# Kernel tuning notes

Measured on AMD Instinct MI355X. Metric: run time of the kernel, lower is better.

Reference implementation:

```python
import jax, jax.numpy as jnp
import numpy as np
import math

HIDDEN = 256
NUM_GAUSSIANS = 64
NUM_FILTERS = 256
CUTOFF = 1.0
COSINE_OFFSET = 0.0
N_NODES = 10000
N_EDGES = 320000


def ssp(x):
    # shifted softplus: softplus(x) - log(2)
    return jax.nn.softplus(x) - jnp.log(2.0).astype(x.dtype)


def setup_inputs() -> dict:
    key = jax.random.key(0)
    ks = jax.random.split(key, 12)

    def xavier(k, fan_out, fan_in):
        a = math.sqrt(6.0 / (fan_in + fan_out))
        return jax.random.uniform(k, (fan_out, fan_in), jnp.float32, -a, a)

    x = jax.random.normal(ks[0], (N_NODES, HIDDEN), jnp.float32)
    ji_pairs = jax.random.randint(ks[1], (2, N_EDGES), 0, N_NODES, jnp.int64)
    e_ji = jax.random.uniform(ks[2], (N_EDGES,), jnp.float32)  # distances in [0, cutoff)
    e_ji_basis = jax.random.normal(ks[3], (N_EDGES, NUM_GAUSSIANS), jnp.float32)

    return {
        "x": x,
        "ji_pairs": ji_pairs,
        "e_ji": e_ji,
        "e_ji_basis": e_ji_basis,
        # filter_nn: Linear(G->F), ssp, Linear(F->F)
        "fw1": xavier(ks[4], NUM_FILTERS, NUM_GAUSSIANS),
        "fb1": jnp.zeros((NUM_FILTERS,), jnp.float32),
        "fw2": xavier(ks[5], NUM_FILTERS, NUM_FILTERS),
        "fb2": jnp.zeros((NUM_FILTERS,), jnp.float32),
        # CFConv linears
        "w1": xavier(ks[6], NUM_FILTERS, HIDDEN),            # linear1, no bias
        "w2": xavier(ks[7], HIDDEN, NUM_FILTERS),            # linear2
        "b2": jnp.zeros((HIDDEN,), jnp.float32),
        # linear3
        "w3": xavier(ks[8], HIDDEN, HIDDEN),
        "b3": jnp.zeros((HIDDEN,), jnp.float32),
    }


def reference(x, ji_pairs, e_ji, e_ji_basis, fw1, fb1, fw2, fb2, w1, w2, b2, w3, b3):
    pi = jnp.asarray(math.pi, x.dtype)
    # cosine cutoff: C = 0.25 * (cos((e - off) * pi / (cutoff - off)) + 1)
    C = 0.25 * (jnp.cos((e_ji - COSINE_OFFSET) * pi / (CUTOFF - COSINE_OFFSET)) + 1.0)
    # filter network on edge RBF features: [E, F]
    W = ssp(e_ji_basis @ fw1.T + fb1) @ fw2.T + fb2
    W = W * C[:, None]
    # linear1 (no bias): [N, F]
    h = x @ w1.T
    # message: x_j * W, gathered from source nodes ji_pairs[0]
    src, dst = ji_pairs[0], ji_pairs[1]
    msg = h[src] * W                                   # [E, F]
    agg = jax.ops.segment_sum(msg, dst, num_segments=x.shape[0])  # [N, F]
    # linear2
    out = agg @ w2.T + b2
    # interaction block tail: act + linear3
    out = ssp(out) @ w3.T + b3
    return out
```

## Files before the change

kernel.cpp:

```cpp
#include <hip/hip_runtime.h>
#include <hip/hip_bf16.h>

typedef __bf16 bf16_t;
typedef float f32x4 __attribute__((ext_vector_type(4)));
typedef __bf16 bf16x8 __attribute__((ext_vector_type(8)));

#define NNODES 10000
#define NEDGES 320000
#define NPAD   10048
#define NPB    8
#define NBLK   (NPAD / NPB)

#define OFF_AGG   256
#define OFF_JIN   (OFF_AGG  + (size_t)NPAD * 256 * 4)
#define OFF_HIST  (OFF_JIN  + (size_t)2 * NEDGES * 4)
#define OFF_CUR   (OFF_HIST + 10240 * 4)
#define OFF_CSR   (OFF_CUR  + 10240 * 4)
#define OFF_PERM  (OFF_CSR  + 10240 * 4)
#define OFF_SRCS  (OFF_PERM + (size_t)NEDGES * 4)
#define OFF_DSTS  (OFF_SRCS + (size_t)NEDGES * 4)
#define OFF_CES   (OFF_DSTS + (size_t)NEDGES * 4)
#define OFF_CE    (OFF_CES  + (size_t)NEDGES * 4)
#define OFF_WB    (OFF_CE   + (size_t)NEDGES * 4)
#define FW1B 0
#define FW2B 16384
#define W1B  81920
#define W2B  147456
#define W3B  212992
#define FB1B 278528
#define FB2B 278784
#define B2B  279040
#define B3B  279296
#define WBN  279552
#define WS_NEED (OFF_WB + (size_t)WBN * 2)
#define OFF_BASC  ((WS_NEED + 255) & ~(size_t)255)
#define WS_NEED_BIG (OFF_BASC + (size_t)NEDGES * 64 * 2)

__device__ __forceinline__ float ssp_f(float v) {
    return fmaxf(v, 0.f) + __logf(1.f + __expf(-fabsf(v))) - 0.69314718055994531f;
}
__device__ __forceinline__ f32x4 mfma16(bf16x8 a, bf16x8 b, f32x4 c) {
    return __builtin_amdgcn_mfma_f32_16x16x32_bf16(a, b, c, 0, 0, 0);
}
template<bool ISB>
__device__ __forceinline__ bf16x8 ld8(const void* p, size_t off) {
    if constexpr (ISB) return *(const bf16x8*)((const bf16_t*)p + off);
    else {
        const float* f = (const float*)p + off;
        f32x4 lo = *(const f32x4*)f, hi = *(const f32x4*)(f + 4);
        bf16x8 r;
        for (int j = 0; j < 4; ++j) { r[j] = (bf16_t)lo[j]; r[j + 4] = (bf16_t)hi[j]; }
        return r;
    }
}
__device__ __forceinline__ bf16x8 ld8r(bool isb, const void* p, size_t off) {
    if (isb) return *(const bf16x8*)((const bf16_t*)p + off);
    const float* f = (const float*)p + off;
    f32x4 lo = *(const f32x4*)f, hi = *(const f32x4*)(f + 4);
    bf16x8 r;
    for (int j = 0; j < 4; ++j) { r[j] = (bf16_t)lo[j]; r[j + 4] = (bf16_t)hi[j]; }
    return r;
}
template<bool ISB>
__device__ __forceinline__ void st1(void* p, size_t off, float v) {
    if constexpr (ISB) ((bf16_t*)p)[off] = (bf16_t)v;
    else               ((float*)p)[off] = v;
}
__device__ __forceinline__ float ld1r(bool isb, const void* p, size_t off) {
    return isb ? (float)((const bf16_t*)p)[off] : ((const float*)p)[off];
}

__global__ __launch_bounds__(256) void detect_kernel(
    const void* __restrict__ x, const int* __restrict__ jraw,
    int* __restrict__ flags, int* __restrict__ hist)
{
    __shared__ int cnt, hi;
    if (threadIdx.x == 0) { cnt = 0; hi = 0; }
    __syncthreads();
    const unsigned short* xw = (const unsigned short*)x;
    int local = 0;
    for (int i = threadIdx.x; i < 2048; i += 256) {
        unsigned int e = (xw[2 * i] >> 7) & 0xFF;
        if (e >= 100 && e <= 141) local++;
    }
    atomicAdd(&cnt, local);
    int v = 0;
    for (int i = threadIdx.x; i < 1024; i += 256) v |= jraw[2 * i + 1];
    if (v != 0) atomicOr(&hi, 1);
    for (int i = threadIdx.x; i < 10240; i += 256) hist[i] = 0;
    __syncthreads();
    if (threadIdx.x == 0) { flags[0] = (cnt > 1024) ? 1 : 0; flags[1] = (hi == 0) ? 1 : 0; }
}

__global__ __launch_bounds__(256) void prep_kernel(
    const int* __restrict__ raw, const int* __restrict__ flags,
    const void* __restrict__ e_ji, const void* __restrict__ basis,
    const void* fw1, const void* fb1, const void* fw2, const void* fb2,
    const void* w1, const void* w2, const void* b2, const void* w3, const void* b3,
    int* __restrict__ jin, int* __restrict__ hist, float* __restrict__ ce,
    bf16_t* __restrict__ wb, bf16_t* __restrict__ basc, int doconv)
{
    const bool is64 = (flags[1] != 0);
    const bool isb  = (flags[0] != 0);
    const int gid = blockIdx.x * 256 + threadIdx.x;
    if (gid < 2 * NEDGES) {
        int iv = is64 ? raw[2 * gid] : raw[gid];
        iv = iv < 0 ? 0 : (iv >= NNODES ? NNODES - 1 : iv);
        jin[gid] = iv;
        if (gid >= NEDGES) atomicAdd(&hist[iv], 1);
    }
    if (gid < NEDGES)
        ce[gid] = 0.25f * (cosf(3.14159265358979f * ld1r(isb, e_ji, gid)) + 1.0f);
    if (gid < WBN) {
        int g = gid; const void* s; int so;
        if      (g < FW2B) { s = fw1; so = g - FW1B; }
        else if (g < W1B)  { s = fw2; so = g - FW2B; }
        else if (g < W2B)  { s = w1;  so = g - W1B; }
        else if (g < W3B)  { s = w2;  so = g - W2B; }
        else if (g < FB1B) { s = w3;  so = g - W3B; }
        else if (g < FB2B) { s = fb1; so = g - FB1B; }
        else if (g < B2B)  { s = fb2; so = g - FB2B; }
        else if (g < B3B)  { s = b2;  so = g - B2B; }
        else               { s = b3;  so = g - B3B; }
        wb[gid] = (bf16_t)ld1r(isb, s, so);
    }
    if (doconv) {
        const int nv = NEDGES * 64 / 8;
        for (int i = gid; i < nv; i += gridDim.x * 256)
            ((bf16x8*)basc)[i] = ld8r(isb, basis, (size_t)i * 8);
    }
}

__global__ __launch_bounds__(256) void scan_kernel(
    const int* __restrict__ hist, int* __restrict__ cur, int* __restrict__ csr)
{
    __shared__ int s[256];
    const int t = threadIdx.x;
    int loc[40]; int sum = 0;
    const int base = t * 40;
    for (int j = 0; j < 40; ++j) {
        int i = base + j;
        loc[j] = (i < NNODES) ? hist[i] : 0;
        sum += loc[j];
    }
    s[t] = sum; __syncthreads();
    for (int off = 1; off < 256; off <<= 1) {
        int v = (t >= off) ? s[t - off] : 0;
        __syncthreads();
        if (t >= off) s[t] += v;
        __syncthreads();
    }
    int pre = (t == 0) ? 0 : s[t - 1];
    for (int j = 0; j < 40; ++j) {
        int i = base + j;
        cur[i] = pre;
        csr[i] = pre;
        pre += loc[j];
    }
}

__global__ __launch_bounds__(256) void scatter_kernel(
    const int* __restrict__ jin, const float* __restrict__ ce,
    int* __restrict__ cur, int* __restrict__ perm,
    int* __restrict__ src_s, int* __restrict__ dst_s, float* __restrict__ ce_s)
{
    int e = blockIdx.x * 256 + threadIdx.x;
    if (e < NEDGES) {
        int d = jin[NEDGES + e];
        int pos = atomicAdd(&cur[d], 1);
        perm[pos]  = e;
        src_s[pos] = jin[e];
        dst_s[pos] = d;
        ce_s[pos]  = ce[e];
    }
}

template<bool ISB>
__global__ __launch_bounds__(256, 2) void h_gemm_kernel(
    const void* __restrict__ x, const bf16_t* __restrict__ wb,
    bf16_t* __restrict__ h, const int* __restrict__ flags)
{
    if ((flags[0] != 0) != ISB) return;
    const bf16_t* w1b = wb + W1B;
    const int w = threadIdx.x >> 6, L = threadIdx.x & 63;
    const int lane16 = L & 15, quad = L >> 4;
    const int nb = blockIdx.x * 64, cb = w * 64;
    f32x4 acc[4][4] = {};
    for (int kc = 0; kc < 8; ++kc) {
        const int ko = kc * 32 + quad * 8;
        bf16x8 af[4], bfr[4];
        for (int mt = 0; mt < 4; ++mt) {
            int row = nb + mt * 16 + lane16;
            if (row >= NNODES) row = NNODES - 1;
            af[mt] = ld8<ISB>(x, (size_t)row * 256 + ko);
        }
        for (int nt = 0; nt < 4; ++nt)
            bfr[nt] = *(const bf16x8*)(w1b + (size_t)(cb + nt * 16 + lane16) * 256 + ko);
        for (int mt = 0; mt < 4; ++mt)
            for (int nt = 0; nt < 4; ++nt)
                acc[mt][nt] = mfma16(af[mt], bfr[nt], acc[mt][nt]);
    }
    for (int mt = 0; mt < 4; ++mt)
        for (int r = 0; r < 4; ++r) {
            int row = nb + mt * 16 + quad * 4 + r;
            if (row < NNODES)
                for (int nt = 0; nt < 4; ++nt)
                    h[(size_t)row * 256 + cb + nt * 16 + lane16] = (bf16_t)acc[mt][nt][r];
        }
}

template<bool ISB, bool CONV>
__global__ __launch_bounds__(256, 3) void edge_kernel(
    const void* __restrict__ basis, const int* __restrict__ csr,
    const int* __restrict__ perm, const int* __restrict__ src_s,
    const int* __restrict__ dst_s, const float* __restrict__ ce_s,
    const bf16_t* __restrict__ wb, const bf16_t* __restrict__ h,
    float* __restrict__ agg, const int* __restrict__ flags)
{
    if (!CONV && (flags[0] != 0) != ISB) return;
    __shared__ bf16_t T[64][264];
    __shared__ float G[NPB][260];
    __shared__ int sperm[64], ssrc[64], snrow[64];
    __shared__ float sce[64];
    const int tid = threadIdx.x;
    const int w = tid >> 6, L = tid & 63;
    const int lane16 = L & 15, quad = L >> 4;
    const int cb = w * 64;
    const int nbase  = blockIdx.x * NPB;
    const int estart = csr[nbase];
    const int eend   = csr[nbase + NPB];

    for (int i = tid; i < NPB * 260; i += 256) (&G[0][0])[i] = 0.f;

    const bf16_t* fw1b = wb + FW1B;
    const bf16_t* fw2b = wb + FW2B;
    float fb1v[4], fb2v[4];
    for (int nt = 0; nt < 4; ++nt) {
        fb1v[nt] = (float)wb[FB1B + cb + nt * 16 + lane16];
        fb2v[nt] = (float)wb[FB2B + cb + nt * 16 + lane16];
    }

    const int hrow = tid >> 2, hseg = tid & 3;

    for (int e0 = estart & ~63; e0 < eend; e0 += 64) {
        __syncthreads();
        {
            int g = tid >> 6, i = tid & 63;
            int e = e0 + i;
            bool valid = (e >= estart) && (e < eend);
            int ee = valid ? e : estart;
            if      (g == 0) sperm[i] = perm[ee];
            else if (g == 1) ssrc[i] = src_s[ee];
            else if (g == 2) {
                int nr = dst_s[ee] - nbase;
                snrow[i] = nr < 0 ? 0 : (nr > NPB - 1 ? NPB - 1 : nr);
            }
            else sce[i] = valid ? ce_s[ee] : 0.f;
        }
        __syncthreads();

        bf16x8 hreg[8];
        {
            const bf16_t* hs = h + (size_t)ssrc[hrow] * 256 + hseg * 64;
            #pragma unroll
            for (int j = 0; j < 8; ++j) hreg[j] = ((const bf16x8*)hs)[j];
        }

        int prow[4];
        for (int mt = 0; mt < 4; ++mt) prow[mt] = sperm[mt * 16 + lane16];

        f32x4 acc1[4][4] = {};
        for (int kc = 0; kc < 2; ++kc) {
            const int ko = kc * 32 + quad * 8;
            bf16x8 af[4], bfr[4];
            for (int mt = 0; mt < 4; ++mt)
                af[mt] = ld8<CONV ? true : ISB>(basis, (size_t)prow[mt] * 64 + ko);
            for (int nt = 0; nt < 4; ++nt)
                bfr[nt] = *(const bf16x8*)(fw1b + (size_t)(cb + nt * 16 + lane16) * 64 + ko);
            for (int mt = 0; mt < 4; ++mt)
                for (int nt = 0; nt < 4; ++nt)
                    acc1[mt][nt] = mfma16(af[mt], bfr[nt], acc1[mt][nt]);
        }
        for (int nt = 0; nt < 4; ++nt) {
            int col = cb + nt * 16 + lane16;
            for (int mt = 0; mt < 4; ++mt)
                for (int r = 0; r < 4; ++r)
                    T[mt * 16 + quad * 4 + r][col] = (bf16_t)ssp_f(acc1[mt][nt][r] + fb1v[nt]);
        }
        __syncthreads();

        f32x4 acc2[4][4] = {};
        for (int kc = 0; kc < 8; ++kc) {
            const int ko = kc * 32 + quad * 8;
            bf16x8 af[4], bfr[4];
            for (int mt = 0; mt < 4; ++mt)
                af[mt] = *(const bf16x8*)(&T[mt * 16 + lane16][ko]);
            for (int nt = 0; nt < 4; ++nt)
                bfr[nt] = *(const bf16x8*)(fw2b + (size_t)(cb + nt * 16 + lane16) * 256 + ko);
            for (int mt = 0; mt < 4; ++mt)
                for (int nt = 0; nt < 4; ++nt)
                    acc2[mt][nt] = mfma16(af[mt], bfr[nt], acc2[mt][nt]);
        }
        __syncthreads();

        {
            bf16_t* dp = &T[hrow][hseg * 64];
            #pragma unroll
            for (int j = 0; j < 8; ++j) ((bf16x8*)dp)[j] = hreg[j];
        }
        __syncthreads();

        float run[4] = {0, 0, 0, 0};
        int curn = -1;
        for (int mt = 0; mt < 4; ++mt)
            for (int r = 0; r < 4; ++r) {
                int row = mt * 16 + quad * 4 + r;
                int nr = snrow[row];
                if (nr != curn) {
                    if (curn >= 0)
                        for (int nt = 0; nt < 4; ++nt)
                            atomicAdd(&G[curn][cb + nt * 16 + lane16], run[nt]);
                    curn = nr;
                    run[0] = run[1] = run[2] = run[3] = 0.f;
                }
                float cv = sce[row];
                for (int nt = 0; nt < 4; ++nt) {
                    int col = cb + nt * 16 + lane16;
                    run[nt] += (acc2[mt][nt][r] + fb2v[nt]) * cv * (float)T[row][col];
                }
            }
        if (curn >= 0)
            for (int nt = 0; nt < 4; ++nt)
                atomicAdd(&G[curn][cb + nt * 16 + lane16], run[nt]);
    }
    __syncthreads();

    for (int n = 0; n < NPB; ++n)
        agg[(size_t)(nbase + n) * 256 + tid] = G[n][tid];
}

template<bool ISB>
__global__ __launch_bounds__(256, 2) void out_kernel(
    const float* __restrict__ agg, const bf16_t* __restrict__ wb,
    void* __restrict__ out, const int* __restrict__ flags)
{
    if ((flags[0] != 0) != ISB) return;
    const bf16_t* w2b = wb + W2B;
    const bf16_t* w3b = wb + W3B;
    __shared__ bf16_t U[64][264];
    const int w = threadIdx.x >> 6, L = threadIdx.x & 63;
    const int lane16 = L & 15, quad = L >> 4;
    const int nb = blockIdx.x * 64, cb = w * 64;

    f32x4 acc[4][4] = {};
    for (int kc = 0; kc < 8; ++kc) {
        const int ko = kc * 32 + quad * 8;
        bf16x8 af[4], bfr[4];
        for (int mt = 0; mt < 4; ++mt) {
            int row = nb + mt * 16 + lane16;
            const float* p = agg + (size_t)row * 256 + ko;
            f32x4 lo = *(const f32x4*)p, hi = *(const f32x4*)(p + 4);
            bf16x8 a;
            for (int j = 0; j < 4; ++j) { a[j] = (bf16_t)lo[j]; a[j + 4] = (bf16_t)hi[j]; }
            af[mt] = a;
        }
        for (int nt = 0; nt < 4; ++nt)
            bfr[nt] = *(const bf16x8*)(w2b + (size_t)(cb + nt * 16 + lane16) * 256 + ko);
        for (int mt = 0; mt < 4; ++mt)
            for (int nt = 0; nt < 4; ++nt)
                acc[mt][nt] = mfma16(af[mt], bfr[nt], acc[mt][nt]);
    }
    for (int nt = 0; nt < 4; ++nt) {
        int col = cb + nt * 16 + lane16;
        float bias = (float)wb[B2B + col];
        for (int mt = 0; mt < 4; ++mt)
            for (int r = 0; r < 4; ++r)
                U[mt * 16 + quad * 4 + r][col] = (bf16_t)ssp_f(acc[mt][nt][r] + bias);
    }
    __syncthreads();

    f32x4 acc2[4][4] = {};
    for (int kc = 0; kc < 8; ++kc) {
        const int ko = kc * 32 + quad * 8;
        bf16x8 af[4], bfr[4];
        for (int mt = 0; mt < 4; ++mt)
            af[mt] = *(const bf16x8*)(&U[mt * 16 + lane16][ko]);
        for (int nt = 0; nt < 4; ++nt)
            bfr[nt] = *(const bf16x8*)(w3b + (size_t)(cb + nt * 16 + lane16) * 256 + ko);
        for (int mt = 0; mt < 4; ++mt)
            for (int nt = 0; nt < 4; ++nt)
                acc2[mt][nt] = mfma16(af[mt], bfr[nt], acc2[mt][nt]);
    }
    for (int mt = 0; mt < 4; ++mt)
        for (int r = 0; r < 4; ++r) {
            int row = nb + mt * 16 + quad * 4 + r;
            if (row < NNODES)
                for (int nt = 0; nt < 4; ++nt) {
                    int col = cb + nt * 16 + lane16;
                    st1<ISB>(out, (size_t)row * 256 + col,
                             acc2[mt][nt][r] + (float)wb[B3B + col]);
                }
        }
}

extern "C" void kernel_launch(void* const* d_in, const int* in_sizes, int n_in,
                              void* d_out, int out_size, void* d_ws, size_t ws_size,
                              hipStream_t stream) {
    const void* x     = d_in[0];
    const int*  ji    = (const int*)d_in[1];
    const void* e_ji  = d_in[2];
    const void* basis = d_in[3];
    const void* fw1   = d_in[4];
    const void* fb1   = d_in[5];
    const void* fw2   = d_in[6];
    const void* fb2   = d_in[7];
    const void* w1    = d_in[8];
    const void* w2    = d_in[9];
    const void* b2    = d_in[10];
    const void* w3    = d_in[11];
    const void* b3    = d_in[12];

    if (ws_size < WS_NEED) return;
    const bool bigws = ws_size >= WS_NEED_BIG;

    char* W = (char*)d_ws;
    int*    flags = (int*)W;
    float*  agg   = (float*)(W + OFF_AGG);
    int*    jin   = (int*)(W + OFF_JIN);
    int*    hist  = (int*)(W + OFF_HIST);
    int*    cur   = (int*)(W + OFF_CUR);
    int*    csr   = (int*)(W + OFF_CSR);
    int*    perm  = (int*)(W + OFF_PERM);
    int*    src_s = (int*)(W + OFF_SRCS);
    int*    dst_s = (int*)(W + OFF_DSTS);
    float*  ce_s  = (float*)(W + OFF_CES);
    float*  ce    = (float*)(W + OFF_CE);
    bf16_t* wb    = (bf16_t*)(W + OFF_WB);
    bf16_t* basc  = (bf16_t*)(W + OFF_BASC);
    bf16_t* h     = (bf16_t*)d_out;

    detect_kernel<<<1, 256, 0, stream>>>(x, ji, flags, hist);
    prep_kernel<<<2500, 256, 0, stream>>>(ji, flags, e_ji, basis, fw1, fb1, fw2, fb2,
                                          w1, w2, b2, w3, b3, jin, hist, ce, wb,
                                          basc, bigws ? 1 : 0);
    scan_kernel<<<1, 256, 0, stream>>>(hist, cur, csr);
    scatter_kernel<<<1250, 256, 0, stream>>>(jin, ce, cur, perm, src_s, dst_s, ce_s);
    h_gemm_kernel<true ><<<157, 256, 0, stream>>>(x, wb, h, flags);
    h_gemm_kernel<false><<<157, 256, 0, stream>>>(x, wb, h, flags);
    if (bigws) {
        edge_kernel<true, true><<<NBLK, 256, 0, stream>>>(basc, csr, perm, src_s, dst_s, ce_s, wb, h, agg, flags);
    } else {
        edge_kernel<true,  false><<<NBLK, 256, 0, stream>>>(basis, csr, perm, src_s, dst_s, ce_s, wb, h, agg, flags);
        edge_kernel<false, false><<<NBLK, 256, 0, stream>>>(basis, csr, perm, src_s, dst_s, ce_s, wb, h, agg, flags);
    }
    out_kernel<true ><<<157, 256, 0, stream>>>(agg, wb, d_out, flags);
    out_kernel<false><<<157, 256, 0, stream>>>(agg, wb, d_out, flags);
}
```

Baseline: 583.7 us.

## Store basis in dst-sorted order and prefetch next edge tile in edge kernel

The scatter kernel now writes the bf16 basis rows in CSR (destination-sorted) order, replacing the separate conversion pass in prep. A new edge_fast_kernel reads those rows contiguously instead of gathering them through perm. It also software-prefetches the next 64-edge tile's basis, src index, dst row, cutoff and h rows into registers while the current tile computes. Each block now handles 16 nodes instead of 8, and blocks with no edges exit early. The costs are higher register pressure, and the scatter's per-edge 128-byte writes land at scattered positions.

New measurement: 633.2 us. 8.5% more time.

```diff
diff --git a/kernel.cpp b/kernel.cpp
--- a/kernel.cpp
+++ b/kernel.cpp
@@ -10,6 +10,8 @@
 #define NPAD   10048
 #define NPB    8
 #define NBLK   (NPAD / NPB)
+#define NPBE   16
+#define NBLKE  (NPAD / NPBE)
 
 #define OFF_AGG   256
 #define OFF_JIN   (OFF_AGG  + (size_t)NPAD * 256 * 4)
@@ -34,7 +36,7 @@
 #define WBN  279552
 #define WS_NEED (OFF_WB + (size_t)WBN * 2)
 #define OFF_BASC  ((WS_NEED + 255) & ~(size_t)255)
-#define WS_NEED_BIG (OFF_BASC + (size_t)NEDGES * 64 * 2)
+#define WS_NEED_BIG (OFF_BASC + (size_t)(NEDGES + 64) * 64 * 2)
 
 __device__ __forceinline__ float ssp_f(float v) {
     return fmaxf(v, 0.f) + __logf(1.f + __expf(-fabsf(v))) - 0.69314718055994531f;
@@ -94,11 +96,11 @@
 
 __global__ __launch_bounds__(256) void prep_kernel(
     const int* __restrict__ raw, const int* __restrict__ flags,
-    const void* __restrict__ e_ji, const void* __restrict__ basis,
+    const void* __restrict__ e_ji,
     const void* fw1, const void* fb1, const void* fw2, const void* fb2,
     const void* w1, const void* w2, const void* b2, const void* w3, const void* b3,
     int* __restrict__ jin, int* __restrict__ hist, float* __restrict__ ce,
-    bf16_t* __restrict__ wb, bf16_t* __restrict__ basc, int doconv)
+    bf16_t* __restrict__ wb)
 {
     const bool is64 = (flags[1] != 0);
     const bool isb  = (flags[0] != 0);
@@ -124,11 +126,6 @@
         else               { s = b3;  so = g - B3B; }
         wb[gid] = (bf16_t)ld1r(isb, s, so);
     }
-    if (doconv) {
-        const int nv = NEDGES * 64 / 8;
-        for (int i = gid; i < nv; i += gridDim.x * 256)
-            ((bf16x8*)basc)[i] = ld8r(isb, basis, (size_t)i * 8);
-    }
 }
 
 __global__ __launch_bounds__(256) void scan_kernel(
@@ -161,17 +158,31 @@
 
 __global__ __launch_bounds__(256) void scatter_kernel(
     const int* __restrict__ jin, const float* __restrict__ ce,
+    const void* __restrict__ basis, const int* __restrict__ flags,
     int* __restrict__ cur, int* __restrict__ perm,
-    int* __restrict__ src_s, int* __restrict__ dst_s, float* __restrict__ ce_s)
+    int* __restrict__ src_s, int* __restrict__ dst_s, float* __restrict__ ce_s,
+    bf16_t* __restrict__ basc, int doconv)
 {
     int e = blockIdx.x * 256 + threadIdx.x;
-    if (e < NEDGES) {
-        int d = jin[NEDGES + e];
-        int pos = atomicAdd(&cur[d], 1);
-        perm[pos]  = e;
-        src_s[pos] = jin[e];
-        dst_s[pos] = d;
-        ce_s[pos]  = ce[e];
+    if (e >= NEDGES) return;
+    int d = jin[NEDGES + e];
+    int pos = atomicAdd(&cur[d], 1);
+    perm[pos]  = e;
+    src_s[pos] = jin[e];
+    dst_s[pos] = d;
+    ce_s[pos]  = ce[e];
+    if (doconv) {
+        const bool isb = (flags[0] != 0);
+        bf16_t* dp = basc + (size_t)pos * 64;
+        if (isb) {
+            #pragma unroll
+            for (int j = 0; j < 8; ++j)
+                *(bf16x8*)(dp + j * 8) = *(const bf16x8*)((const bf16_t*)basis + (size_t)e * 64 + j * 8);
+        } else {
+            #pragma unroll
+            for (int j = 0; j < 8; ++j)
+                *(bf16x8*)(dp + j * 8) = ld8r(false, basis, (size_t)e * 64 + j * 8);
+        }
     }
 }
 
@@ -209,28 +220,33 @@
         }
 }
 
-template<bool ISB, bool CONV>
-__global__ __launch_bounds__(256, 3) void edge_kernel(
-    const void* __restrict__ basis, const int* __restrict__ csr,
-    const int* __restrict__ perm, const int* __restrict__ src_s,
-    const int* __restrict__ dst_s, const float* __restrict__ ce_s,
+__global__ __launch_bounds__(256, 3) void edge_fast_kernel(
+    const bf16_t* __restrict__ basc, const int* __restrict__ csr,
+    const int* __restrict__ src_s, const int* __restrict__ dst_s,
+    const float* __restrict__ ce_s,
     const bf16_t* __restrict__ wb, const bf16_t* __restrict__ h,
-    float* __restrict__ agg, const int* __restrict__ flags)
-{
-    if (!CONV && (flags[0] != 0) != ISB) return;
+    float* __restrict__ agg)
+{
     __shared__ bf16_t T[64][264];
-    __shared__ float G[NPB][260];
-    __shared__ int sperm[64], ssrc[64], snrow[64];
+    __shared__ float G[NPBE][260];
+    __shared__ int snrow[64];
     __shared__ float sce[64];
     const int tid = threadIdx.x;
     const int w = tid >> 6, L = tid & 63;
     const int lane16 = L & 15, quad = L >> 4;
     const int cb = w * 64;
-    const int nbase  = blockIdx.x * NPB;
+    const int nbase  = blockIdx.x * NPBE;
     const int estart = csr[nbase];
-    const int eend   = csr[nbase + NPB];
-
-    for (int i = tid; i < NPB * 260; i += 256) (&G[0][0])[i] = 0.f;
+    const int eend   = csr[nbase + NPBE];
+
+    for (int i = tid; i < NPBE * 260; i += 256) (&G[0][0])[i] = 0.f;
+
+    if (estart >= eend) {
+        __syncthreads();
+        for (int n = 0; n < NPBE; ++n)
+            agg[(size_t)(nbase + n) * 256 + tid] = 0.f;
+        return;
+    }
 
     const bf16_t* fw1b = wb + FW1B;
     const bf16_t* fw2b = wb + FW2B;
@@ -241,51 +257,79 @@
     }
 
     const int hrow = tid >> 2, hseg = tid & 3;
-
-    for (int e0 = estart & ~63; e0 < eend; e0 += 64) {
-        __syncthreads();
-        {
-            int g = tid >> 6, i = tid & 63;
-            int e = e0 + i;
+    const int e0first = estart & ~63;
+
+    int mrow = 0; float mce = 0.f; int msrc;
+    bf16x8 breg[2][4];
+    bf16x8 hreg[8];
+
+    {
+        int e = e0first + L;
+        int ec = e < NEDGES - 1 ? e : NEDGES - 1;
+        if (w == 0) {
             bool valid = (e >= estart) && (e < eend);
-            int ee = valid ? e : estart;
-            if      (g == 0) sperm[i] = perm[ee];
-            else if (g == 1) ssrc[i] = src_s[ee];
-            else if (g == 2) {
-                int nr = dst_s[ee] - nbase;
-                snrow[i] = nr < 0 ? 0 : (nr > NPB - 1 ? NPB - 1 : nr);
+            int nr = dst_s[ec] - nbase;
+            mrow = nr < 0 ? 0 : (nr > NPBE - 1 ? NPBE - 1 : nr);
+            mce  = valid ? ce_s[ec] : 0.f;
+        }
+        int eh = e0first + hrow; eh = eh < NEDGES - 1 ? eh : NEDGES - 1;
+        msrc = src_s[eh];
+        #pragma unroll
+        for (int kc = 0; kc < 2; ++kc)
+            #pragma unroll
+            for (int mt = 0; mt < 4; ++mt) {
+                int er = e0first + mt * 16 + lane16;
+                er = er < NEDGES - 1 ? er : NEDGES - 1;
+                breg[kc][mt] = *(const bf16x8*)(basc + (size_t)er * 64 + kc * 32 + quad * 8);
             }
-            else sce[i] = valid ? ce_s[ee] : 0.f;
-        }
-        __syncthreads();
-
-        bf16x8 hreg[8];
-        {
-            const bf16_t* hs = h + (size_t)ssrc[hrow] * 256 + hseg * 64;
-            #pragma unroll
-            for (int j = 0; j < 8; ++j) hreg[j] = ((const bf16x8*)hs)[j];
-        }
-
-        int prow[4];
-        for (int mt = 0; mt < 4; ++mt) prow[mt] = sperm[mt * 16 + lane16];
+        const bf16_t* hs = h + (size_t)msrc * 256 + hseg * 64;
+        #pragma unroll
+        for (int j = 0; j < 8; ++j) hreg[j] = ((const bf16x8*)hs)[j];
+    }
+
+    for (int e0 = e0first; e0 < eend; e0 += 64) {
+        const int e0n = e0 + 64;
+        const bool more = e0n < eend;
+        __syncthreads();
+        if (w == 0) { snrow[L] = mrow; sce[L] = mce; }
 
         f32x4 acc1[4][4] = {};
+        #pragma unroll
         for (int kc = 0; kc < 2; ++kc) {
             const int ko = kc * 32 + quad * 8;
-            bf16x8 af[4], bfr[4];
-            for (int mt = 0; mt < 4; ++mt)
-                af[mt] = ld8<CONV ? true : ISB>(basis, (size_t)prow[mt] * 64 + ko);
+            bf16x8 bfr[4];
             for (int nt = 0; nt < 4; ++nt)
                 bfr[nt] = *(const bf16x8*)(fw1b + (size_t)(cb + nt * 16 + lane16) * 64 + ko);
             for (int mt = 0; mt < 4; ++mt)
                 for (int nt = 0; nt < 4; ++nt)
-                    acc1[mt][nt] = mfma16(af[mt], bfr[nt], acc1[mt][nt]);
+                    acc1[mt][nt] = mfma16(breg[kc][mt], bfr[nt], acc1[mt][nt]);
         }
         for (int nt = 0; nt < 4; ++nt) {
             int col = cb + nt * 16 + lane16;
             for (int mt = 0; mt < 4; ++mt)
                 for (int r = 0; r < 4; ++r)
                     T[mt * 16 + quad * 4 + r][col] = (bf16_t)ssp_f(acc1[mt][nt][r] + fb1v[nt]);
+        }
+
+        if (more) {
+            int e = e0n + L;
+            int ec = e < NEDGES - 1 ? e : NEDGES - 1;
+            if (w == 0) {
+                bool valid = e < eend;
+                int nr = dst_s[ec] - nbase;
+                mrow = nr < 0 ? 0 : (nr > NPBE - 1 ? NPBE - 1 : nr);
+                mce  = valid ? ce_s[ec] : 0.f;
+            }
+            int eh = e0n + hrow; eh = eh < NEDGES - 1 ? eh : NEDGES - 1;
+            msrc = src_s[eh];
+            #pragma unroll
+            for (int kc = 0; kc < 2; ++kc)
+                #pragma unroll
+                for (int mt = 0; mt < 4; ++mt) {
+                    int er = e0n + mt * 16 + lane16;
+                    er = er < NEDGES - 1 ? er : NEDGES - 1;
+                    breg[kc][mt] = *(const bf16x8*)(basc + (size_t)er * 64 + kc * 32 + quad * 8);
+                }
         }
         __syncthreads();
 
@@ -309,6 +353,12 @@
             for (int j = 0; j < 8; ++j) ((bf16x8*)dp)[j] = hreg[j];
         }
         __syncthreads();
+
+        if (more) {
+            const bf16_t* hs = h + (size_t)msrc * 256 + hseg * 64;
+            #pragma unroll
+            for (int j = 0; j < 8; ++j) hreg[j] = ((const bf16x8*)hs)[j];
+        }
 
         float run[4] = {0, 0, 0, 0};
         int curn = -1;
@@ -335,6 +385,136 @@
     }
     __syncthreads();
 
+    for (int n = 0; n < NPBE; ++n)
+        agg[(size_t)(nbase + n) * 256 + tid] = G[n][tid];
+}
+
+template<bool ISB>
+__global__ __launch_bounds__(256, 3) void edge_kernel(
+    const void* __restrict__ basis, const int* __restrict__ csr,
+    const int* __restrict__ perm, const int* __restrict__ src_s,
+    const int* __restrict__ dst_s, const float* __restrict__ ce_s,
+    const bf16_t* __restrict__ wb, const bf16_t* __restrict__ h,
+    float* __restrict__ agg, const int* __restrict__ flags)
+{
+    if ((flags[0] != 0) != ISB) return;
+    __shared__ bf16_t T[64][264];
+    __shared__ float G[NPB][260];
+    __shared__ int sperm[64], ssrc[64], snrow[64];
+    __shared__ float sce[64];
+    const int tid = threadIdx.x;
+    const int w = tid >> 6, L = tid & 63;
+    const int lane16 = L & 15, quad = L >> 4;
+    const int cb = w * 64;
+    const int nbase  = blockIdx.x * NPB;
+    const int estart = csr[nbase];
+    const int eend   = csr[nbase + NPB];
+
+    for (int i = tid; i < NPB * 260; i += 256) (&G[0][0])[i] = 0.f;
+
+    const bf16_t* fw1b = wb + FW1B;
+    const bf16_t* fw2b = wb + FW2B;
+    float fb1v[4], fb2v[4];
+    for (int nt = 0; nt < 4; ++nt) {
+        fb1v[nt] = (float)wb[FB1B + cb + nt * 16 + lane16];
+        fb2v[nt] = (float)wb[FB2B + cb + nt * 16 + lane16];
+    }
+
+    const int hrow = tid >> 2, hseg = tid & 3;
+
+    for (int e0 = estart & ~63; e0 < eend; e0 += 64) {
+        __syncthreads();
+        {
+            int g = tid >> 6, i = tid & 63;
+            int e = e0 + i;
+            bool valid = (e >= estart) && (e < eend);
+            int ee = valid ? e : estart;
+            if      (g == 0) sperm[i] = perm[ee];
+            else if (g == 1) ssrc[i] = src_s[ee];
+            else if (g == 2) {
+                int nr = dst_s[ee] - nbase;
+                snrow[i] = nr < 0 ? 0 : (nr > NPB - 1 ? NPB - 1 : nr);
+            }
+            else sce[i] = valid ? ce_s[ee] : 0.f;
+        }
+        __syncthreads();
+
+        bf16x8 hreg[8];
+        {
+            const bf16_t* hs = h + (size_t)ssrc[hrow] * 256 + hseg * 64;
+            #pragma unroll
+            for (int j = 0; j < 8; ++j) hreg[j] = ((const bf16x8*)hs)[j];
+        }
+
+        int prow[4];
+        for (int mt = 0; mt < 4; ++mt) prow[mt] = sperm[mt * 16 + lane16];
+
+        f32x4 acc1[4][4] = {};
+        for (int kc = 0; kc < 2; ++kc) {
+            const int ko = kc * 32 + quad * 8;
+            bf16x8 af[4], bfr[4];
+            for (int mt = 0; mt < 4; ++mt)
+                af[mt] = ld8<ISB>(basis, (size_t)prow[mt] * 64 + ko);
+            for (int nt = 0; nt < 4; ++nt)
+                bfr[nt] = *(const bf16x8*)(fw1b + (size_t)(cb + nt * 16 + lane16) * 64 + ko);
+            for (int mt = 0; mt < 4; ++mt)
+                for (int nt = 0; nt < 4; ++nt)
+                    acc1[mt][nt] = mfma16(af[mt], bfr[nt], acc1[mt][nt]);
+        }
+        for (int nt = 0; nt < 4; ++nt) {
+            int col = cb + nt * 16 + lane16;
+            for (int mt = 0; mt < 4; ++mt)
+                for (int r = 0; r < 4; ++r)
+                    T[mt * 16 + quad * 4 + r][col] = (bf16_t)ssp_f(acc1[mt][nt][r] + fb1v[nt]);
+        }
+        __syncthreads();
+
+        f32x4 acc2[4][4] = {};
+        for (int kc = 0; kc < 8; ++kc) {
+            const int ko = kc * 32 + quad * 8;
+            bf16x8 af[4], bfr[4];
+            for (int mt = 0; mt < 4; ++mt)
+                af[mt] = *(const bf16x8*)(&T[mt * 16 + lane16][ko]);
+            for (int nt = 0; nt < 4; ++nt)
+                bfr[nt] = *(const bf16x8*)(fw2b + (size_t)(cb + nt * 16 + lane16) * 256 + ko);
+            for (int mt = 0; mt < 4; ++mt)
+                for (int nt = 0; nt < 4; ++nt)
+                    acc2[mt][nt] = mfma16(af[mt], bfr[nt], acc2[mt][nt]);
+        }
+        __syncthreads();
+
+        {
+            bf16_t* dp = &T[hrow][hseg * 64];
+            #pragma unroll
+            for (int j = 0; j < 8; ++j) ((bf16x8*)dp)[j] = hreg[j];
+        }
+        __syncthreads();
+
+        float run[4] = {0, 0, 0, 0};
+        int curn = -1;
+        for (int mt = 0; mt < 4; ++mt)
+            for (int r = 0; r < 4; ++r) {
+                int row = mt * 16 + quad * 4 + r;
+                int nr = snrow[row];
+                if (nr != curn) {
+                    if (curn >= 0)
+                        for (int nt = 0; nt < 4; ++nt)
+                            atomicAdd(&G[curn][cb + nt * 16 + lane16], run[nt]);
+                    curn = nr;
+                    run[0] = run[1] = run[2] = run[3] = 0.f;
+                }
+                float cv = sce[row];
+                for (int nt = 0; nt < 4; ++nt) {
+                    int col = cb + nt * 16 + lane16;
+                    run[nt] += (acc2[mt][nt][r] + fb2v[nt]) * cv * (float)T[row][col];
+                }
+            }
+        if (curn >= 0)
+            for (int nt = 0; nt < 4; ++nt)
+                atomicAdd(&G[curn][cb + nt * 16 + lane16], run[nt]);
+    }
+    __syncthreads();
+
     for (int n = 0; n < NPB; ++n)
         agg[(size_t)(nbase + n) * 256 + tid] = G[n][tid];
 }
@@ -440,18 +620,18 @@
     bf16_t* h     = (bf16_t*)d_out;
 
     detect_kernel<<<1, 256, 0, stream>>>(x, ji, flags, hist);
-    prep_kernel<<<2500, 256, 0, stream>>>(ji, flags, e_ji, basis, fw1, fb1, fw2, fb2,
-                                          w1, w2, b2, w3, b3, jin, hist, ce, wb,
-                                          basc, bigws ? 1 : 0);
+    prep_kernel<<<2500, 256, 0, stream>>>(ji, flags, e_ji, fw1, fb1, fw2, fb2,
+                                          w1, w2, b2, w3, b3, jin, hist, ce, wb);
     scan_kernel<<<1, 256, 0, stream>>>(hist, cur, csr);
-    scatter_kernel<<<1250, 256, 0, stream>>>(jin, ce, cur, perm, src_s, dst_s, ce_s);
+    scatter_kernel<<<1250, 256, 0, stream>>>(jin, ce, basis, flags, cur, perm,
+                                             src_s, dst_s, ce_s, basc, bigws ? 1 : 0);
     h_gemm_kernel<true ><<<157, 256, 0, stream>>>(x, wb, h, flags);
     h_gemm_kernel<false><<<157, 256, 0, stream>>>(x, wb, h, flags);
     if (bigws) {
-        edge_kernel<true, true><<<NBLK, 256, 0, stream>>>(basc, csr, perm, src_s, dst_s, ce_s, wb, h, agg, flags);
+        edge_fast_kernel<<<NBLKE, 256, 0, stream>>>(basc, csr, src_s, dst_s, ce_s, wb, h, agg);
     } else {
-        edge_kernel<true,  false><<<NBLK, 256, 0, stream>>>(basis, csr, perm, src_s, dst_s, ce_s, wb, h, agg, flags);
-        edge_kernel<false, false><<<NBLK, 256, 0, stream>>>(basis, csr, perm, src_s, dst_s, ce_s, wb, h, agg, flags);
+        edge_kernel<true ><<<NBLK, 256, 0, stream>>>(basis, csr, perm, src_s, dst_s, ce_s, wb, h, agg, flags);
+        edge_kernel<false><<<NBLK, 256, 0, stream>>>(basis, csr, perm, src_s, dst_s, ce_s, wb, h, agg, flags);
     }
     out_kernel<true ><<<157, 256, 0, stream>>>(agg, wb, d_out, flags);
     out_kernel<false><<<157, 256, 0, stream>>>(agg, wb, d_out, flags);
```

## Parallelize edge kernel over fixed 64-edge chunks with global atomics

Applied to the files above, without the earlier changes.

The edge kernel no longer gives each block a group of 8 destination nodes that it walks through edge tile by edge tile. Each block now handles exactly one 64-edge tile of the dst-sorted edge list and adds run-length partial sums straight into global agg with atomics. agg is now zeroed in prep_kernel, and the bf16 pre-conversion of the basis into a workspace copy is removed. This evens out load across blocks, removes the per-block loop, the shared accumulator and the partial-tile waste, and raises occupancy to 4 blocks. The cost is global float atomics on contention at node boundaries and always reading the basis in its original format.

Result: faster. 525.8 us (-9.9%).

```diff
diff --git a/kernel.cpp b/kernel.cpp
--- a/kernel.cpp
+++ b/kernel.cpp
@@ -8,8 +8,7 @@
 #define NNODES 10000
 #define NEDGES 320000
 #define NPAD   10048
-#define NPB    8
-#define NBLK   (NPAD / NPB)
+#define NB2    (NEDGES / 64)
 
 #define OFF_AGG   256
 #define OFF_JIN   (OFF_AGG  + (size_t)NPAD * 256 * 4)
@@ -33,8 +32,6 @@
 #define B3B  279296
 #define WBN  279552
 #define WS_NEED (OFF_WB + (size_t)WBN * 2)
-#define OFF_BASC  ((WS_NEED + 255) & ~(size_t)255)
-#define WS_NEED_BIG (OFF_BASC + (size_t)NEDGES * 64 * 2)
 
 __device__ __forceinline__ float ssp_f(float v) {
     return fmaxf(v, 0.f) + __logf(1.f + __expf(-fabsf(v))) - 0.69314718055994531f;
@@ -53,14 +50,6 @@
         return r;
     }
 }
-__device__ __forceinline__ bf16x8 ld8r(bool isb, const void* p, size_t off) {
-    if (isb) return *(const bf16x8*)((const bf16_t*)p + off);
-    const float* f = (const float*)p + off;
-    f32x4 lo = *(const f32x4*)f, hi = *(const f32x4*)(f + 4);
-    bf16x8 r;
-    for (int j = 0; j < 4; ++j) { r[j] = (bf16_t)lo[j]; r[j + 4] = (bf16_t)hi[j]; }
-    return r;
-}
 template<bool ISB>
 __device__ __forceinline__ void st1(void* p, size_t off, float v) {
     if constexpr (ISB) ((bf16_t*)p)[off] = (bf16_t)v;
@@ -94,11 +83,11 @@
 
 __global__ __launch_bounds__(256) void prep_kernel(
     const int* __restrict__ raw, const int* __restrict__ flags,
-    const void* __restrict__ e_ji, const void* __restrict__ basis,
+    const void* __restrict__ e_ji,
     const void* fw1, const void* fb1, const void* fw2, const void* fb2,
     const void* w1, const void* w2, const void* b2, const void* w3, const void* b3,
     int* __restrict__ jin, int* __restrict__ hist, float* __restrict__ ce,
-    bf16_t* __restrict__ wb, bf16_t* __restrict__ basc, int doconv)
+    bf16_t* __restrict__ wb, float* __restrict__ agg)
 {
     const bool is64 = (flags[1] != 0);
     const bool isb  = (flags[0] != 0);
@@ -124,11 +113,9 @@
         else               { s = b3;  so = g - B3B; }
         wb[gid] = (bf16_t)ld1r(isb, s, so);
     }
-    if (doconv) {
-        const int nv = NEDGES * 64 / 8;
-        for (int i = gid; i < nv; i += gridDim.x * 256)
-            ((bf16x8*)basc)[i] = ld8r(isb, basis, (size_t)i * 8);
-    }
+    f32x4 z = {0.f, 0.f, 0.f, 0.f};
+    for (int i = gid; i < NPAD * 256 / 4; i += 2500 * 256)
+        ((f32x4*)agg)[i] = z;
 }
 
 __global__ __launch_bounds__(256) void scan_kernel(
@@ -209,28 +196,30 @@
         }
 }
 
-template<bool ISB, bool CONV>
-__global__ __launch_bounds__(256, 3) void edge_kernel(
-    const void* __restrict__ basis, const int* __restrict__ csr,
-    const int* __restrict__ perm, const int* __restrict__ src_s,
-    const int* __restrict__ dst_s, const float* __restrict__ ce_s,
+template<bool ISB>
+__global__ __launch_bounds__(256, 4) void edge_kernel2(
+    const void* __restrict__ basis, const int* __restrict__ perm,
+    const int* __restrict__ src_s, const int* __restrict__ dst_s,
+    const float* __restrict__ ce_s,
     const bf16_t* __restrict__ wb, const bf16_t* __restrict__ h,
     float* __restrict__ agg, const int* __restrict__ flags)
 {
-    if (!CONV && (flags[0] != 0) != ISB) return;
+    if ((flags[0] != 0) != ISB) return;
     __shared__ bf16_t T[64][264];
-    __shared__ float G[NPB][260];
-    __shared__ int sperm[64], ssrc[64], snrow[64];
+    __shared__ int sperm[64], ssrc[64], sdst[64];
     __shared__ float sce[64];
     const int tid = threadIdx.x;
     const int w = tid >> 6, L = tid & 63;
     const int lane16 = L & 15, quad = L >> 4;
     const int cb = w * 64;
-    const int nbase  = blockIdx.x * NPB;
-    const int estart = csr[nbase];
-    const int eend   = csr[nbase + NPB];
-
-    for (int i = tid; i < NPB * 260; i += 256) (&G[0][0])[i] = 0.f;
+    const int e0 = blockIdx.x * 64;
+
+    {
+        if      (w == 0) sperm[L] = perm[e0 + L];
+        else if (w == 1) ssrc[L] = src_s[e0 + L];
+        else if (w == 2) sdst[L] = dst_s[e0 + L];
+        else             sce[L]  = ce_s[e0 + L];
+    }
 
     const bf16_t* fw1b = wb + FW1B;
     const bf16_t* fw2b = wb + FW2B;
@@ -239,104 +228,82 @@
         fb1v[nt] = (float)wb[FB1B + cb + nt * 16 + lane16];
         fb2v[nt] = (float)wb[FB2B + cb + nt * 16 + lane16];
     }
+    __syncthreads();
 
     const int hrow = tid >> 2, hseg = tid & 3;
-
-    for (int e0 = estart & ~63; e0 < eend; e0 += 64) {
-        __syncthreads();
-        {
-            int g = tid >> 6, i = tid & 63;
-            int e = e0 + i;
-            bool valid = (e >= estart) && (e < eend);
-            int ee = valid ? e : estart;
-            if      (g == 0) sperm[i] = perm[ee];
-            else if (g == 1) ssrc[i] = src_s[ee];
-            else if (g == 2) {
-                int nr = dst_s[ee] - nbase;
-                snrow[i] = nr < 0 ? 0 : (nr > NPB - 1 ? NPB - 1 : nr);
+    bf16x8 hreg[8];
+    {
+        const bf16_t* hs = h + (size_t)ssrc[hrow] * 256 + hseg * 64;
+        #pragma unroll
+        for (int j = 0; j < 8; ++j) hreg[j] = ((const bf16x8*)hs)[j];
+    }
+
+    int prow[4];
+    for (int mt = 0; mt < 4; ++mt) prow[mt] = sperm[mt * 16 + lane16];
+
+    f32x4 acc1[4][4] = {};
+    for (int kc = 0; kc < 2; ++kc) {
+        const int ko = kc * 32 + quad * 8;
+        bf16x8 af[4], bfr[4];
+        for (int mt = 0; mt < 4; ++mt)
+            af[mt] = ld8<ISB>(basis, (size_t)prow[mt] * 64 + ko);
+        for (int nt = 0; nt < 4; ++nt)
+            bfr[nt] = *(const bf16x8*)(fw1b + (size_t)(cb + nt * 16 + lane16) * 64 + ko);
+        for (int mt = 0; mt < 4; ++mt)
+            for (int nt = 0; nt < 4; ++nt)
+                acc1[mt][nt] = mfma16(af[mt], bfr[nt], acc1[mt][nt]);
+    }
+    for (int nt = 0; nt < 4; ++nt) {
+        int col = cb + nt * 16 + lane16;
+        for (int mt = 0; mt < 4; ++mt)
+            for (int r = 0; r < 4; ++r)
+                T[mt * 16 + quad * 4 + r][col] = (bf16_t)ssp_f(acc1[mt][nt][r] + fb1v[nt]);
+    }
+    __syncthreads();
+
+    f32x4 acc2[4][4] = {};
+    for (int kc = 0; kc < 8; ++kc) {
+        const int ko = kc * 32 + quad * 8;
+        bf16x8 af[4], bfr[4];
+        for (int mt = 0; mt < 4; ++mt)
+            af[mt] = *(const bf16x8*)(&T[mt * 16 + lane16][ko]);
+        for (int nt = 0; nt < 4; ++nt)
+            bfr[nt] = *(const bf16x8*)(fw2b + (size_t)(cb + nt * 16 + lane16) * 256 + ko);
+        for (int mt = 0; mt < 4; ++mt)
+            for (int nt = 0; nt < 4; ++nt)
+                acc2[mt][nt] = mfma16(af[mt], bfr[nt], acc2[mt][nt]);
+    }
+    __syncthreads();
+
+    {
+        bf16_t* dp = &T[hrow][hseg * 64];
+        #pragma unroll
+        for (int j = 0; j < 8; ++j) ((bf16x8*)dp)[j] = hreg[j];
+    }
+    __syncthreads();
+
+    float run[4] = {0, 0, 0, 0};
+    int curn = -1;
+    for (int mt = 0; mt < 4; ++mt)
+        for (int r = 0; r < 4; ++r) {
+            int row = mt * 16 + quad * 4 + r;
+            int n = sdst[row];
+            if (n != curn) {
+                if (curn >= 0)
+                    for (int nt = 0; nt < 4; ++nt)
+                        atomicAdd(&agg[(size_t)curn * 256 + cb + nt * 16 + lane16], run[nt]);
+                curn = n;
+                run[0] = run[1] = run[2] = run[3] = 0.f;
             }
-            else sce[i] = valid ? ce_s[ee] : 0.f;
+            float cv = sce[row];
+            for (int nt = 0; nt < 4; ++nt) {
+                int col = cb + nt * 16 + lane16;
+                run[nt] += (acc2[mt][nt][r] + fb2v[nt]) * cv * (float)T[row][col];
+            }
         }
-        __syncthreads();
-
-        bf16x8 hreg[8];
-        {
-            const bf16_t* hs = h + (size_t)ssrc[hrow] * 256 + hseg * 64;
-            #pragma unroll
-            for (int j = 0; j < 8; ++j) hreg[j] = ((const bf16x8*)hs)[j];
-        }
-
-        int prow[4];
-        for (int mt = 0; mt < 4; ++mt) prow[mt] = sperm[mt * 16 + lane16];
-
-        f32x4 acc1[4][4] = {};
-        for (int kc = 0; kc < 2; ++kc) {
-            const int ko = kc * 32 + quad * 8;
-            bf16x8 af[4], bfr[4];
-            for (int mt = 0; mt < 4; ++mt)
-                af[mt] = ld8<CONV ? true : ISB>(basis, (size_t)prow[mt] * 64 + ko);
-            for (int nt = 0; nt < 4; ++nt)
-                bfr[nt] = *(const bf16x8*)(fw1b + (size_t)(cb + nt * 16 + lane16) * 64 + ko);
-            for (int mt = 0; mt < 4; ++mt)
-                for (int nt = 0; nt < 4; ++nt)
-                    acc1[mt][nt] = mfma16(af[mt], bfr[nt], acc1[mt][nt]);
-        }
-        for (int nt = 0; nt < 4; ++nt) {
-            int col = cb + nt * 16 + lane16;
-            for (int mt = 0; mt < 4; ++mt)
-                for (int r = 0; r < 4; ++r)
-                    T[mt * 16 + quad * 4 + r][col] = (bf16_t)ssp_f(acc1[mt][nt][r] + fb1v[nt]);
-        }
-        __syncthreads();
-
-        f32x4 acc2[4][4] = {};
-        for (int kc = 0; kc < 8; ++kc) {
-            const int ko = kc * 32 + quad * 8;
-            bf16x8 af[4], bfr[4];
-            for (int mt = 0; mt < 4; ++mt)
-                af[mt] = *(const bf16x8*)(&T[mt * 16 + lane16][ko]);
-            for (int nt = 0; nt < 4; ++nt)
-                bfr[nt] = *(const bf16x8*)(fw2b + (size_t)(cb + nt * 16 + lane16) * 256 + ko);
-            for (int mt = 0; mt < 4; ++mt)
-                for (int nt = 0; nt < 4; ++nt)
-                    acc2[mt][nt] = mfma16(af[mt], bfr[nt], acc2[mt][nt]);
-        }
-        __syncthreads();
-
-        {
-            bf16_t* dp = &T[hrow][hseg * 64];
-            #pragma unroll
-            for (int j = 0; j < 8; ++j) ((bf16x8*)dp)[j] = hreg[j];
-        }
-        __syncthreads();
-
-        float run[4] = {0, 0, 0, 0};
-        int curn = -1;
-        for (int mt = 0; mt < 4; ++mt)
-            for (int r = 0; r < 4; ++r) {
-                int row = mt * 16 + quad * 4 + r;
-                int nr = snrow[row];
-                if (nr != curn) {
-                    if (curn >= 0)
-                        for (int nt = 0; nt < 4; ++nt)
-                            atomicAdd(&G[curn][cb + nt * 16 + lane16], run[nt]);
-                    curn = nr;
-                    run[0] = run[1] = run[2] = run[3] = 0.f;
-                }
-                float cv = sce[row];
-                for (int nt = 0; nt < 4; ++nt) {
-                    int col = cb + nt * 16 + lane16;
-                    run[nt] += (acc2[mt][nt][r] + fb2v[nt]) * cv * (float)T[row][col];
-                }
-            }
-        if (curn >= 0)
-            for (int nt = 0; nt < 4; ++nt)
-                atomicAdd(&G[curn][cb + nt * 16 + lane16], run[nt]);
-    }
-    __syncthreads();
-
-    for (int n = 0; n < NPB; ++n)
-        agg[(size_t)(nbase + n) * 256 + tid] = G[n][tid];
+    if (curn >= 0)
+        for (int nt = 0; nt < 4; ++nt)
+            atomicAdd(&agg[(size_t)curn * 256 + cb + nt * 16 + lane16], run[nt]);
 }
 
 template<bool ISB>
@@ -421,7 +388,6 @@
     const void* b3    = d_in[12];
 
     if (ws_size < WS_NEED) return;
-    const bool bigws = ws_size >= WS_NEED_BIG;
 
     char* W = (char*)d_ws;
     int*    flags = (int*)W;
@@ -436,23 +402,17 @@
     float*  ce_s  = (float*)(W + OFF_CES);
     float*  ce    = (float*)(W + OFF_CE);
     bf16_t* wb    = (bf16_t*)(W + OFF_WB);
-    bf16_t* basc  = (bf16_t*)(W + OFF_BASC);
     bf16_t* h     = (bf16_t*)d_out;
 
     detect_kernel<<<1, 256, 0, stream>>>(x, ji, flags, hist);
-    prep_kernel<<<2500, 256, 0, stream>>>(ji, flags, e_ji, basis, fw1, fb1, fw2, fb2,
-                                          w1, w2, b2, w3, b3, jin, hist, ce, wb,
-                                          basc, bigws ? 1 : 0);
+    prep_kernel<<<2500, 256, 0, stream>>>(ji, flags, e_ji, fw1, fb1, fw2, fb2,
+                                          w1, w2, b2, w3, b3, jin, hist, ce, wb, agg);
     scan_kernel<<<1, 256, 0, stream>>>(hist, cur, csr);
     scatter_kernel<<<1250, 256, 0, stream>>>(jin, ce, cur, perm, src_s, dst_s, ce_s);
     h_gemm_kernel<true ><<<157, 256, 0, stream>>>(x, wb, h, flags);
     h_gemm_kernel<false><<<157, 256, 0, stream>>>(x, wb, h, flags);
-    if (bigws) {
-        edge_kernel<true, true><<<NBLK, 256, 0, stream>>>(basc, csr, perm, src_s, dst_s, ce_s, wb, h, agg, flags);
-    } else {
-        edge_kernel<true,  false><<<NBLK, 256, 0, stream>>>(basis, csr, perm, src_s, dst_s, ce_s, wb, h, agg, flags);
-        edge_kernel<false, false><<<NBLK, 256, 0, stream>>>(basis, csr, perm, src_s, dst_s, ce_s, wb, h, agg, flags);
-    }
+    edge_kernel2<true ><<<NB2, 256, 0, stream>>>(basis, perm, src_s, dst_s, ce_s, wb, h, agg, flags);
+    edge_kernel2<false><<<NB2, 256, 0, stream>>>(basis, perm, src_s, dst_s, ce_s, wb, h, agg, flags);
     out_kernel<true ><<<157, 256, 0, stream>>>(agg, wb, d_out, flags);
     out_kernel<false><<<157, 256, 0, stream>>>(agg, wb, d_out, flags);
 }
```
